# Optimization experiments

Measured on AMD Instinct MI355X. Metric: run time of the kernel, lower is better.

Reference implementation:

```python
import jax, jax.numpy as jnp
import numpy as np

# Model dims
B, S, H, E, I, K = 2, 2048, 1024, 8, 1024, 2
ALPHA, LIMIT = 1.702, 7.0  # gpt_oss activation constants (module defaults)


def setup_inputs() -> dict:
    key = jax.random.key(0)
    ks = jax.random.split(key, 5)
    sc = 0.02
    return {
        "hidden_states": jax.random.normal(ks[0], (B, S, H), jnp.float32),
        "router_weight": jax.random.normal(ks[1], (H, E), jnp.float32) * sc,
        "gate_up_proj": jax.random.normal(ks[2], (E, H, 2 * I), jnp.float32) * sc,
        "gate_up_proj_bias": jnp.zeros((E, 2 * I), jnp.float32),
        "down_proj": jax.random.normal(ks[3], (E, I, H), jnp.float32) * sc,
        "down_proj_bias": jnp.zeros((E, H), jnp.float32),
    }


def reference(hidden_states, router_weight, gate_up_proj, gate_up_proj_bias,
              down_proj, down_proj_bias):
    Bt, St, Ht = hidden_states.shape
    x = hidden_states.reshape(-1, Ht)           # [T, H], T = B*S
    T = x.shape[0]

    # Router: linear -> top-k -> softmax over selected logits (gpt_oss style)
    logits = x @ router_weight                  # [T, E]
    top_vals, top_idx = jax.lax.top_k(logits, K)
    scores = jax.nn.softmax(top_vals, axis=-1)  # [T, K]
    # Sparse combine weights: w[t, e] = score if e selected for t, else 0
    w = jnp.zeros((T, E), x.dtype).at[jnp.arange(T)[:, None], top_idx].set(scores)

    # Fused gate+up projection for every expert (dense equivalent of grouped GEMM;
    # unselected experts get zero combine weight so math matches sparse path)
    gu = jnp.einsum('th,ehf->tef', x, gate_up_proj) + gate_up_proj_bias  # [T, E, 2I]
    gate = gu[..., ::2]                         # interleaved gate (default)
    up = gu[..., 1::2]
    gate = jnp.minimum(gate, LIMIT)
    up = jnp.clip(up, -LIMIT, LIMIT)
    glu = gate * jax.nn.sigmoid(gate * ALPHA)
    act = (up + 1.0) * glu                      # [T, E, I]

    down = jnp.einsum('tei,eih->teh', act, down_proj) + down_proj_bias  # [T, E, H]

    # Weighted combine over experts (all-to-all combine is identity at D=1)
    out = jnp.einsum('te,teh->th', w, down)     # [T, H]
    return out.reshape(Bt, St, Ht)
```

## Files before the change

kernel.cpp:

```cpp
#include <hip/hip_runtime.h>
#include <hip/hip_bf16.h>
#include <cstdint>
#include <cstddef>

constexpr int T_TOK = 4096;
constexpr int H_DIM = 1024;
constexpr int E_NUM = 8;
constexpr int I_DIM = 1024;
constexpr int F2    = 2048;
constexpr float ALPHA = 1.702f;
constexpr float LIMIT = 7.0f;
constexpr int BM = 128;
constexpr int BK = 32;
constexpr int NT = 32;
constexpr int MAXT = 72;

using u16    = unsigned short;
using bf16x8 = __attribute__((ext_vector_type(8))) __bf16;
using s16x8  = __attribute__((ext_vector_type(8))) short;
using f32x4  = __attribute__((ext_vector_type(4))) float;

constexpr size_t WS_W1T  = 0;
constexpr size_t WS_DOWN = 0;
constexpr size_t WS_W2T  = 33554432;
constexpr size_t WS_ACT  = 50331648;
constexpr size_t WS_ETOK = 67108864;
constexpr size_t WS_POS  = 67239936;
constexpr size_t WS_CNT  = 67272704;
constexpr size_t WS_ROWB = 67272736;
constexpr size_t WS_ASGN = 67272768;
constexpr size_t WS_TOPE = 67273792;
constexpr size_t WS_TOPW = 67290176;
constexpr size_t WS_XBF  = 67322944;
constexpr size_t WS_NEED = 75711552;

__device__ __forceinline__ u16 f2bf(float f) {
    union { float f; unsigned u; } v; v.f = f;
    return (u16)((v.u + 0x7FFFu + ((v.u >> 16) & 1u)) >> 16);
}
__device__ __forceinline__ float bf2f(u16 u) {
    union { unsigned u; float f; } v; v.u = (unsigned)u << 16; return v.f;
}

__device__ __forceinline__ s16x8 pack8(float4 a, float4 b) {
    s16x8 r;
    r[0] = (short)f2bf(a.x); r[1] = (short)f2bf(a.y);
    r[2] = (short)f2bf(a.z); r[3] = (short)f2bf(a.w);
    r[4] = (short)f2bf(b.x); r[5] = (short)f2bf(b.y);
    r[6] = (short)f2bf(b.z); r[7] = (short)f2bf(b.w);
    return r;
}

__device__ __forceinline__ void gload16(const void* g, void* l) {
    __builtin_amdgcn_global_load_lds((const __attribute__((address_space(1))) unsigned*)g,
                                     (__attribute__((address_space(3))) unsigned*)l,
                                     16, 0, 0);
}

__device__ __forceinline__ void pipe_sync() {
    __builtin_amdgcn_sched_barrier(0);
    asm volatile("s_waitcnt vmcnt(0) lgkmcnt(0)" ::: "memory");
    __builtin_amdgcn_s_barrier();
    __builtin_amdgcn_sched_barrier(0);
}

__global__ __launch_bounds__(256) void k_xbf(const float* __restrict__ x,
                                             u16* __restrict__ xbf) {
    const size_t i = ((size_t)blockIdx.x * 256 + threadIdx.x) * 8;
    float4 a = *(const float4*)(x + i);
    float4 b = *(const float4*)(x + i + 4);
    *(s16x8*)(xbf + i) = pack8(a, b);
}

__global__ __launch_bounds__(256) void k_transpose_w1(const float* __restrict__ in,
                                                      u16* __restrict__ out) {
    __shared__ float tile[64][65];
    const int e = blockIdx.z, c0 = blockIdx.x * 64, h0 = blockIdx.y * 64;
    const int tid = threadIdx.x;
    const float* src = in + ((size_t)e * H_DIM + h0) * F2 + c0;
#pragma unroll
    for (int i = 0; i < 4; ++i) {
        int r = (tid >> 4) + i * 16, c = (tid & 15) * 4;
        float4 v = *(const float4*)(src + (size_t)r * F2 + c);
        tile[r][c] = v.x; tile[r][c + 1] = v.y; tile[r][c + 2] = v.z; tile[r][c + 3] = v.w;
    }
    __syncthreads();
    const int c = tid >> 2, hseg = (tid & 3) * 16;
    const int g = c & 1;
    const int f = (c0 + c) >> 1;
    u16* dst = out + (((size_t)e * 2 + g) * I_DIM + f) * H_DIM + h0 + hseg;
    s16x8 o0, o1;
#pragma unroll
    for (int j = 0; j < 8; ++j) o0[j] = (short)f2bf(tile[hseg + j][c]);
#pragma unroll
    for (int j = 0; j < 8; ++j) o1[j] = (short)f2bf(tile[hseg + 8 + j][c]);
    *(s16x8*)dst = o0;
    *(s16x8*)(dst + 8) = o1;
}

__global__ __launch_bounds__(256) void k_transpose_w2(const float* __restrict__ in,
                                                      u16* __restrict__ out) {
    __shared__ float tile[64][65];
    const int e = blockIdx.z, h0 = blockIdx.x * 64, i0 = blockIdx.y * 64;
    const int tid = threadIdx.x;
    const float* src = in + ((size_t)e * I_DIM + i0) * H_DIM + h0;
#pragma unroll
    for (int i = 0; i < 4; ++i) {
        int r = (tid >> 4) + i * 16, c = (tid & 15) * 4;
        float4 v = *(const float4*)(src + (size_t)r * H_DIM + c);
        tile[r][c] = v.x; tile[r][c + 1] = v.y; tile[r][c + 2] = v.z; tile[r][c + 3] = v.w;
    }
    __syncthreads();
    const int c = tid >> 2, iseg = (tid & 3) * 16;
    u16* dst = out + ((size_t)e * H_DIM + h0 + c) * I_DIM + i0 + iseg;
    s16x8 o0, o1;
#pragma unroll
    for (int j = 0; j < 8; ++j) o0[j] = (short)f2bf(tile[iseg + j][c]);
#pragma unroll
    for (int j = 0; j < 8; ++j) o1[j] = (short)f2bf(tile[iseg + 8 + j][c]);
    *(s16x8*)dst = o0;
    *(s16x8*)(dst + 8) = o1;
}

__global__ __launch_bounds__(256) void k_router_top2(const float* __restrict__ x,
                                                     const float* __restrict__ rw,
                                                     int* __restrict__ tope,
                                                     float2* __restrict__ topw) {
    const int wave = threadIdx.x >> 6, lane = threadIdx.x & 63;
    const int t = blockIdx.x * 4 + wave;
    const float* xr = x + (size_t)t * H_DIM;
    float acc[E_NUM];
#pragma unroll
    for (int e = 0; e < E_NUM; ++e) acc[e] = 0.f;
    for (int h = lane; h < H_DIM; h += 64) {
        float xv = xr[h];
        const float* r = rw + h * E_NUM;
#pragma unroll
        for (int e = 0; e < E_NUM; ++e) acc[e] += xv * r[e];
    }
#pragma unroll
    for (int e = 0; e < E_NUM; ++e) {
        float v = acc[e];
#pragma unroll
        for (int o = 32; o > 0; o >>= 1) v += __shfl_down(v, o);
        acc[e] = v;
    }
    if (lane == 0) {
        int e0 = 0; float v0 = acc[0];
#pragma unroll
        for (int e = 1; e < E_NUM; ++e) if (acc[e] > v0) { v0 = acc[e]; e0 = e; }
        int e1 = -1; float v1 = -3.4e38f;
#pragma unroll
        for (int e = 0; e < E_NUM; ++e) if (e != e0 && acc[e] > v1) { v1 = acc[e]; e1 = e; }
        float ew = expf(v1 - v0);
        float inv = 1.f / (1.f + ew);
        tope[t] = e0 | (e1 << 8);
        topw[t] = make_float2(inv, ew * inv);
    }
}

__global__ __launch_bounds__(256) void k_router_scatter(const int* __restrict__ tope,
                                                        int* __restrict__ cnt,
                                                        int* __restrict__ ent_tok,
                                                        int2* __restrict__ pos) {
    __shared__ int lcnt[E_NUM];
    __shared__ int gbase[E_NUM];
    const int tid = threadIdx.x;
    const int t = blockIdx.x * 256 + tid;
    if (tid < E_NUM) lcnt[tid] = 0;
    __syncthreads();
    const int pk = tope[t];
    const int e0 = pk & 0xff, e1 = pk >> 8;
    const int o0 = atomicAdd(&lcnt[e0], 1);
    const int o1 = atomicAdd(&lcnt[e1], 1);
    __syncthreads();
    if (tid < E_NUM) gbase[tid] = atomicAdd(&cnt[tid], lcnt[tid]);
    __syncthreads();
    const int p0 = gbase[e0] + o0;
    const int p1 = gbase[e1] + o1;
    ent_tok[e0 * T_TOK + p0] = t;
    ent_tok[e1 * T_TOK + p1] = t;
    pos[t] = make_int2(p0, p1);
}

__global__ void k_schedule(const int* __restrict__ cnt, int* __restrict__ rowbase,
                           int* __restrict__ assign) {
    if (threadIdx.x == 0) {
        int rb = 0, na = 0;
        for (int e = 0; e < E_NUM; ++e) {
            rowbase[e] = rb;
            int nt = (cnt[e] + BM - 1) >> 7;
            for (int m = 0; m < nt; ++m) assign[na++] = (e << 16) | m;
            rb += cnt[e];
        }
        for (; na < MAXT; ++na) assign[na] = -1;
    }
}

__global__ __launch_bounds__(256, 4) void k_gemm1(
    const u16* __restrict__ xbf, const u16* __restrict__ w1t,
    const float* __restrict__ bias, const int* __restrict__ ent_tok,
    const int* __restrict__ cnt, const int* __restrict__ rowbase,
    const int* __restrict__ assign, u16* __restrict__ act) {
    const int a = assign[blockIdx.y];
    if (a < 0) return;
    const int e = a >> 16, mt = a & 0xffff;
    const int j0 = blockIdx.x * 64;
    const int cs = cnt[e], r0 = mt * BM;
    __shared__ __align__(16) u16 As[2][BM * BK];
    __shared__ __align__(16) u16 Bs[2][BM * BK];
    const int tid = threadIdx.x, lane = tid & 63, wv = tid >> 6;
    const int lr = lane >> 2;
    const int sm = (lane & 3) ^ ((lr >> 1) & 3);
    const u16* asrc[2]; const u16* bsrc[2]; int dofs[2];
#pragma unroll
    for (int j = 0; j < 2; ++j) {
        const int row = wv * 32 + j * 16 + lr;
        const int aent = r0 + row;
        const int tok = (aent < cs) ? ent_tok[e * T_TOK + aent] : 0;
        asrc[j] = xbf + (size_t)tok * H_DIM + sm * 8;
        const int g = row >> 6;
        const int f = j0 + (row & 63);
        bsrc[j] = w1t + (((size_t)e * 2 + g) * I_DIM + f) * H_DIM + sm * 8;
        dofs[j] = (wv * 32 + j * 16) * BK;
    }
    const int wm = wv >> 1, wn = wv & 1;
    const int lcol = lane & 15, lk = lane >> 4;
    int aoff[4], goff[2], uoff[2];
#pragma unroll
    for (int mi = 0; mi < 4; ++mi) {
        const int r = wm * 64 + mi * 16 + lcol;
        aoff[mi] = r * 64 + ((lk ^ ((r >> 1) & 3)) << 4);
    }
#pragma unroll
    for (int nj = 0; nj < 2; ++nj) {
        const int rg_ = wn * 32 + nj * 16 + lcol;
        const int ru  = 64 + rg_;
        goff[nj] = rg_ * 64 + ((lk ^ ((rg_ >> 1) & 3)) << 4);
        uoff[nj] = ru  * 64 + ((lk ^ ((ru  >> 1) & 3)) << 4);
    }
    f32x4 ag[4][2], au[4][2];
    const f32x4 z = {0.f, 0.f, 0.f, 0.f};
#pragma unroll
    for (int mi = 0; mi < 4; ++mi) { ag[mi][0] = z; ag[mi][1] = z; au[mi][0] = z; au[mi][1] = z; }
#pragma unroll
    for (int j = 0; j < 2; ++j) {
        gload16(asrc[j], &As[0][dofs[j]]);
        gload16(bsrc[j], &Bs[0][dofs[j]]);
    }
    pipe_sync();
    int cur = 0;
    for (int t = 0; t < NT; ++t) {
        if (t + 1 < NT) {
            const int kn = (t + 1) * BK;
            u16* Ad = As[cur ^ 1]; u16* Bd = Bs[cur ^ 1];
#pragma unroll
            for (int j = 0; j < 2; ++j) {
                gload16(asrc[j] + kn, Ad + dofs[j]);
                gload16(bsrc[j] + kn, Bd + dofs[j]);
            }
        }
        const char* Ab = (const char*)As[cur];
        const char* Bb = (const char*)Bs[cur];
        bf16x8 af[4];
#pragma unroll
        for (int mi = 0; mi < 4; ++mi) af[mi] = *(const bf16x8*)(Ab + aoff[mi]);
        const bf16x8 g0 = *(const bf16x8*)(Bb + goff[0]);
        const bf16x8 g1 = *(const bf16x8*)(Bb + goff[1]);
        const bf16x8 u0 = *(const bf16x8*)(Bb + uoff[0]);
        const bf16x8 u1 = *(const bf16x8*)(Bb + uoff[1]);
#pragma unroll
        for (int mi = 0; mi < 4; ++mi) {
            ag[mi][0] = __builtin_amdgcn_mfma_f32_16x16x32_bf16(af[mi], g0, ag[mi][0], 0, 0, 0);
            au[mi][0] = __builtin_amdgcn_mfma_f32_16x16x32_bf16(af[mi], u0, au[mi][0], 0, 0, 0);
            ag[mi][1] = __builtin_amdgcn_mfma_f32_16x16x32_bf16(af[mi], g1, ag[mi][1], 0, 0, 0);
            au[mi][1] = __builtin_amdgcn_mfma_f32_16x16x32_bf16(af[mi], u1, au[mi][1], 0, 0, 0);
        }
        pipe_sync();
        cur ^= 1;
    }
    const int rbase = rowbase[e];
#pragma unroll
    for (int mi = 0; mi < 4; ++mi) {
#pragma unroll
        for (int nj = 0; nj < 2; ++nj) {
            const int col = j0 + wn * 32 + nj * 16 + lcol;
            const float bg_ = bias[e * F2 + 2 * col];
            const float bu_ = bias[e * F2 + 2 * col + 1];
#pragma unroll
            for (int rg = 0; rg < 4; ++rg) {
                const int r = wm * 64 + mi * 16 + lk * 4 + rg;
                if (r0 + r < cs) {
                    float gv = ag[mi][nj][rg] + bg_;
                    float uv = au[mi][nj][rg] + bu_;
                    gv = fminf(gv, LIMIT);
                    uv = fminf(fmaxf(uv, -LIMIT), LIMIT);
                    const float glu = gv / (1.f + expf(-ALPHA * gv));
                    act[(size_t)(rbase + r0 + r) * I_DIM + col] = f2bf((uv + 1.f) * glu);
                }
            }
        }
    }
}

__global__ __launch_bounds__(256, 4) void k_gemm2(
    const u16* __restrict__ act, const u16* __restrict__ w2t,
    const int* __restrict__ cnt, const int* __restrict__ rowbase,
    const int* __restrict__ assign, u16* __restrict__ down) {
    const int a = assign[blockIdx.y];
    if (a < 0) return;
    const int e = a >> 16, mt = a & 0xffff;
    const int n0 = blockIdx.x * 128;
    const int cs = cnt[e], r0 = mt * BM, rbase = rowbase[e];
    __shared__ __align__(16) u16 As[2][BM * BK];
    __shared__ __align__(16) u16 Bs[2][BM * BK];
    const int tid = threadIdx.x, lane = tid & 63, wv = tid >> 6;
    const int lr = lane >> 2;
    const int sm = (lane & 3) ^ ((lr >> 1) & 3);
    const u16* asrc[2]; const u16* bsrc[2]; int dofs[2];
#pragma unroll
    for (int j = 0; j < 2; ++j) {
        const int row = wv * 32 + j * 16 + lr;
        int ar = rbase + r0 + row;
        if (ar > 2 * T_TOK - 1) ar = 2 * T_TOK - 1;
        asrc[j] = act + (size_t)ar * I_DIM + sm * 8;
        bsrc[j] = w2t + ((size_t)e * H_DIM + n0 + row) * I_DIM + sm * 8;
        dofs[j] = (wv * 32 + j * 16) * BK;
    }
    const int wm = wv >> 1, wn = wv & 1;
    const int lcol = lane & 15, lk = lane >> 4;
    int aoff[4], boff[4];
#pragma unroll
    for (int mi = 0; mi < 4; ++mi) {
        const int r = wm * 64 + mi * 16 + lcol;
        const int b = wn * 64 + mi * 16 + lcol;
        aoff[mi] = r * 64 + ((lk ^ ((r >> 1) & 3)) << 4);
        boff[mi] = b * 64 + ((lk ^ ((b >> 1) & 3)) << 4);
    }
    f32x4 acc[4][4];
    const f32x4 z = {0.f, 0.f, 0.f, 0.f};
#pragma unroll
    for (int mi = 0; mi < 4; ++mi)
#pragma unroll
        for (int nj = 0; nj < 4; ++nj) acc[mi][nj] = z;
#pragma unroll
    for (int j = 0; j < 2; ++j) {
        gload16(asrc[j], &As[0][dofs[j]]);
        gload16(bsrc[j], &Bs[0][dofs[j]]);
    }
    pipe_sync();
    int cur = 0;
    for (int t = 0; t < NT; ++t) {
        if (t + 1 < NT) {
            const int kn = (t + 1) * BK;
            u16* Ad = As[cur ^ 1]; u16* Bd = Bs[cur ^ 1];
#pragma unroll
            for (int j = 0; j < 2; ++j) {
                gload16(asrc[j] + kn, Ad + dofs[j]);
                gload16(bsrc[j] + kn, Bd + dofs[j]);
            }
        }
        const char* Ab = (const char*)As[cur];
        const char* Bb = (const char*)Bs[cur];
        bf16x8 af[4], bf_[4];
#pragma unroll
        for (int mi = 0; mi < 4; ++mi) af[mi]  = *(const bf16x8*)(Ab + aoff[mi]);
#pragma unroll
        for (int nj = 0; nj < 4; ++nj) bf_[nj] = *(const bf16x8*)(Bb + boff[nj]);
#pragma unroll
        for (int mi = 0; mi < 4; ++mi)
#pragma unroll
            for (int nj = 0; nj < 4; ++nj)
                acc[mi][nj] = __builtin_amdgcn_mfma_f32_16x16x32_bf16(af[mi], bf_[nj], acc[mi][nj], 0, 0, 0);
        pipe_sync();
        cur ^= 1;
    }
#pragma unroll
    for (int mi = 0; mi < 4; ++mi) {
#pragma unroll
        for (int nj = 0; nj < 4; ++nj) {
            const int col = n0 + wn * 64 + nj * 16 + lcol;
#pragma unroll
            for (int rg = 0; rg < 4; ++rg) {
                const int r = wm * 64 + mi * 16 + lk * 4 + rg;
                if (r0 + r < cs)
                    down[(size_t)(rbase + r0 + r) * H_DIM + col] = f2bf(acc[mi][nj][rg]);
            }
        }
    }
}

__global__ __launch_bounds__(256) void k_combine(
    const int* __restrict__ tope, const float2* __restrict__ topw,
    const int2* __restrict__ pos, const int* __restrict__ rowb,
    const float* __restrict__ b2, const u16* __restrict__ down,
    float* __restrict__ out) {
    const int t = blockIdx.x;
    const int c = threadIdx.x * 4;
    const int pk = tope[t];
    const int e0 = pk & 0xff, e1 = pk >> 8;
    const int2 pp = pos[t];
    const float2 w = topw[t];
    const size_t ro0 = (size_t)(rowb[e0] + pp.x) * H_DIM;
    const size_t ro1 = (size_t)(rowb[e1] + pp.y) * H_DIM;
    ushort4 d0 = *(const ushort4*)(down + ro0 + c);
    ushort4 d1 = *(const ushort4*)(down + ro1 + c);
    float4 bb0 = *(const float4*)(b2 + e0 * H_DIM + c);
    float4 bb1 = *(const float4*)(b2 + e1 * H_DIM + c);
    float4 o;
    o.x = w.x * (bf2f(d0.x) + bb0.x) + w.y * (bf2f(d1.x) + bb1.x);
    o.y = w.x * (bf2f(d0.y) + bb0.y) + w.y * (bf2f(d1.y) + bb1.y);
    o.z = w.x * (bf2f(d0.z) + bb0.z) + w.y * (bf2f(d1.z) + bb1.z);
    o.w = w.x * (bf2f(d0.w) + bb0.w) + w.y * (bf2f(d1.w) + bb1.w);
    *(float4*)(out + (size_t)t * H_DIM + c) = o;
}

extern "C" void kernel_launch(void* const* d_in, const int* in_sizes, int n_in,
                              void* d_out, int out_size, void* d_ws, size_t ws_size,
                              hipStream_t stream) {
    const float* x   = (const float*)d_in[0];
    const float* rw  = (const float*)d_in[1];
    const float* w1  = (const float*)d_in[2];
    const float* b1  = (const float*)d_in[3];
    const float* w2  = (const float*)d_in[4];
    const float* b2  = (const float*)d_in[5];
    float* out = (float*)d_out;
    char* ws = (char*)d_ws;

    if (ws_size < WS_NEED) return;

    u16*    W1T  = (u16*)(ws + WS_W1T);
    u16*    DOWN = (u16*)(ws + WS_DOWN);
    u16*    W2T  = (u16*)(ws + WS_W2T);
    u16*    ACT  = (u16*)(ws + WS_ACT);
    int*    ETOK = (int*)(ws + WS_ETOK);
    int2*   POS  = (int2*)(ws + WS_POS);
    int*    CNT  = (int*)(ws + WS_CNT);
    int*    ROWB = (int*)(ws + WS_ROWB);
    int*    ASGN = (int*)(ws + WS_ASGN);
    int*    TOPE = (int*)(ws + WS_TOPE);
    float2* TOPW = (float2*)(ws + WS_TOPW);
    u16*    XBF  = (u16*)(ws + WS_XBF);

    hipMemsetAsync(CNT, 0, E_NUM * sizeof(int), stream);

    k_xbf<<<T_TOK * H_DIM / 2048, 256, 0, stream>>>(x, XBF);
    k_transpose_w1<<<dim3(32, 16, 8), 256, 0, stream>>>(w1, W1T);
    k_transpose_w2<<<dim3(16, 16, 8), 256, 0, stream>>>(w2, W2T);
    k_router_top2<<<T_TOK / 4, 256, 0, stream>>>(x, rw, TOPE, TOPW);
    k_router_scatter<<<T_TOK / 256, 256, 0, stream>>>(TOPE, CNT, ETOK, POS);
    k_schedule<<<1, 64, 0, stream>>>(CNT, ROWB, ASGN);
    k_gemm1<<<dim3(16, MAXT), 256, 0, stream>>>(XBF, W1T, b1, ETOK, CNT, ROWB, ASGN, ACT);
    k_gemm2<<<dim3(8, MAXT), 256, 0, stream>>>(ACT, W2T, CNT, ROWB, ASGN, DOWN);
    k_combine<<<T_TOK, 256, 0, stream>>>(TOPE, TOPW, POS, ROWB, b2, DOWN, out);
}
```

Measured before the change: 165.2 us.

## Make MoE GEMMs persistent with atomic job queue and triple-buffered loads

```diff
diff --git a/kernel.cpp b/kernel.cpp
--- a/kernel.cpp
+++ b/kernel.cpp
@@ -14,6 +14,8 @@
 constexpr int BK = 32;
 constexpr int NT = 32;
 constexpr int MAXT = 72;
+constexpr int NJOB1 = 16 * MAXT;
+constexpr int NJOB2 = 8 * MAXT;
 
 using u16    = unsigned short;
 using bf16x8 = __attribute__((ext_vector_type(8))) __bf16;
@@ -29,6 +31,7 @@
 constexpr size_t WS_CNT  = 67272704;
 constexpr size_t WS_ROWB = 67272736;
 constexpr size_t WS_ASGN = 67272768;
+constexpr size_t WS_JC   = 67273280;
 constexpr size_t WS_TOPE = 67273792;
 constexpr size_t WS_TOPW = 67290176;
 constexpr size_t WS_XBF  = 67322944;
@@ -57,12 +60,9 @@
                                      16, 0, 0);
 }
 
-__device__ __forceinline__ void pipe_sync() {
-    __builtin_amdgcn_sched_barrier(0);
-    asm volatile("s_waitcnt vmcnt(0) lgkmcnt(0)" ::: "memory");
-    __builtin_amdgcn_s_barrier();
-    __builtin_amdgcn_sched_barrier(0);
-}
+#define SB0() __builtin_amdgcn_sched_barrier(0)
+#define BARC() do { SB0(); __builtin_amdgcn_s_barrier(); SB0(); } while (0)
+#define WVM(n) do { SB0(); asm volatile("s_waitcnt vmcnt(" #n ")" ::: "memory"); } while (0)
 
 __global__ __launch_bounds__(256) void k_xbf(const float* __restrict__ x,
                                              u16* __restrict__ xbf) {
@@ -197,36 +197,21 @@
     }
 }
 
-__global__ __launch_bounds__(256, 4) void k_gemm1(
+__global__ __launch_bounds__(256, 3) void k_gemm1(
     const u16* __restrict__ xbf, const u16* __restrict__ w1t,
     const float* __restrict__ bias, const int* __restrict__ ent_tok,
     const int* __restrict__ cnt, const int* __restrict__ rowbase,
-    const int* __restrict__ assign, u16* __restrict__ act) {
-    const int a = assign[blockIdx.y];
-    if (a < 0) return;
-    const int e = a >> 16, mt = a & 0xffff;
-    const int j0 = blockIdx.x * 64;
-    const int cs = cnt[e], r0 = mt * BM;
-    __shared__ __align__(16) u16 As[2][BM * BK];
-    __shared__ __align__(16) u16 Bs[2][BM * BK];
+    const int* __restrict__ assign, int* __restrict__ jc,
+    u16* __restrict__ act) {
+    __shared__ __align__(16) u16 As[3][BM * BK];
+    __shared__ __align__(16) u16 Bs[3][BM * BK];
+    __shared__ int jobsh;
     const int tid = threadIdx.x, lane = tid & 63, wv = tid >> 6;
     const int lr = lane >> 2;
     const int sm = (lane & 3) ^ ((lr >> 1) & 3);
-    const u16* asrc[2]; const u16* bsrc[2]; int dofs[2];
-#pragma unroll
-    for (int j = 0; j < 2; ++j) {
-        const int row = wv * 32 + j * 16 + lr;
-        const int aent = r0 + row;
-        const int tok = (aent < cs) ? ent_tok[e * T_TOK + aent] : 0;
-        asrc[j] = xbf + (size_t)tok * H_DIM + sm * 8;
-        const int g = row >> 6;
-        const int f = j0 + (row & 63);
-        bsrc[j] = w1t + (((size_t)e * 2 + g) * I_DIM + f) * H_DIM + sm * 8;
-        dofs[j] = (wv * 32 + j * 16) * BK;
-    }
     const int wm = wv >> 1, wn = wv & 1;
     const int lcol = lane & 15, lk = lane >> 4;
-    int aoff[4], goff[2], uoff[2];
+    int aoff[4], goff[2], uoff[2], dofs[2];
 #pragma unroll
     for (int mi = 0; mi < 4; ++mi) {
         const int r = wm * 64 + mi * 16 + lcol;
@@ -239,97 +224,123 @@
         goff[nj] = rg_ * 64 + ((lk ^ ((rg_ >> 1) & 3)) << 4);
         uoff[nj] = ru  * 64 + ((lk ^ ((ru  >> 1) & 3)) << 4);
     }
-    f32x4 ag[4][2], au[4][2];
-    const f32x4 z = {0.f, 0.f, 0.f, 0.f};
-#pragma unroll
-    for (int mi = 0; mi < 4; ++mi) { ag[mi][0] = z; ag[mi][1] = z; au[mi][0] = z; au[mi][1] = z; }
-#pragma unroll
-    for (int j = 0; j < 2; ++j) {
-        gload16(asrc[j], &As[0][dofs[j]]);
-        gload16(bsrc[j], &Bs[0][dofs[j]]);
-    }
-    pipe_sync();
-    int cur = 0;
-    for (int t = 0; t < NT; ++t) {
-        if (t + 1 < NT) {
-            const int kn = (t + 1) * BK;
-            u16* Ad = As[cur ^ 1]; u16* Bd = Bs[cur ^ 1];
-#pragma unroll
-            for (int j = 0; j < 2; ++j) {
-                gload16(asrc[j] + kn, Ad + dofs[j]);
-                gload16(bsrc[j] + kn, Bd + dofs[j]);
+#pragma unroll
+    for (int j = 0; j < 2; ++j) dofs[j] = (wv * 32 + j * 16) * BK;
+
+    for (;;) {
+        if (tid == 0) jobsh = atomicAdd(jc, 1);
+        __syncthreads();
+        const int job = jobsh;
+        __syncthreads();
+        if (job >= NJOB1) break;
+        const int pan = job & 15, ti = job >> 4;
+        const int a = assign[ti];
+        if (a < 0) continue;
+        const int e = a >> 16, mt = a & 0xffff;
+        const int j0 = pan * 64;
+        const int cs = cnt[e], r0 = mt * BM, rbase = rowbase[e];
+
+        const u16* asrc[2]; const u16* bsrc[2];
+#pragma unroll
+        for (int j = 0; j < 2; ++j) {
+            const int row = wv * 32 + j * 16 + lr;
+            const int aent = r0 + row;
+            const int tok = (aent < cs) ? ent_tok[e * T_TOK + aent] : 0;
+            asrc[j] = xbf + (size_t)tok * H_DIM + sm * 8;
+            const int g = row >> 6;
+            const int f = j0 + (row & 63);
+            bsrc[j] = w1t + (((size_t)e * 2 + g) * I_DIM + f) * H_DIM + sm * 8;
+        }
+        f32x4 ag[4][2], au[4][2];
+        const f32x4 z = {0.f, 0.f, 0.f, 0.f};
+#pragma unroll
+        for (int mi = 0; mi < 4; ++mi) { ag[mi][0] = z; ag[mi][1] = z; au[mi][0] = z; au[mi][1] = z; }
+
+        u16 *Ar = As[0], *An = As[1], *Af = As[2];
+        u16 *Br = Bs[0], *Bn = Bs[1], *Bf = Bs[2];
+#pragma unroll
+        for (int j = 0; j < 2; ++j) {
+            gload16(asrc[j], Ar + dofs[j]);
+            gload16(bsrc[j], Br + dofs[j]);
+        }
+#pragma unroll
+        for (int j = 0; j < 2; ++j) {
+            gload16(asrc[j] + BK, An + dofs[j]);
+            gload16(bsrc[j] + BK, Bn + dofs[j]);
+        }
+        for (int t = 0; t < NT; ++t) {
+            if (t + 2 < NT) {
+                const int kn = (t + 2) * BK;
+#pragma unroll
+                for (int j = 0; j < 2; ++j) {
+                    gload16(asrc[j] + kn, Af + dofs[j]);
+                    gload16(bsrc[j] + kn, Bf + dofs[j]);
+                }
+                WVM(8);
+            } else if (t + 1 < NT) {
+                WVM(4);
+            } else {
+                WVM(0);
             }
-        }
-        const char* Ab = (const char*)As[cur];
-        const char* Bb = (const char*)Bs[cur];
-        bf16x8 af[4];
-#pragma unroll
-        for (int mi = 0; mi < 4; ++mi) af[mi] = *(const bf16x8*)(Ab + aoff[mi]);
-        const bf16x8 g0 = *(const bf16x8*)(Bb + goff[0]);
-        const bf16x8 g1 = *(const bf16x8*)(Bb + goff[1]);
-        const bf16x8 u0 = *(const bf16x8*)(Bb + uoff[0]);
-        const bf16x8 u1 = *(const bf16x8*)(Bb + uoff[1]);
+            BARC();
+            const char* Ab = (const char*)Ar;
+            const char* Bb = (const char*)Br;
+            bf16x8 af[4];
+#pragma unroll
+            for (int mi = 0; mi < 4; ++mi) af[mi] = *(const bf16x8*)(Ab + aoff[mi]);
+            const bf16x8 g0 = *(const bf16x8*)(Bb + goff[0]);
+            const bf16x8 g1 = *(const bf16x8*)(Bb + goff[1]);
+            const bf16x8 u0 = *(const bf16x8*)(Bb + uoff[0]);
+            const bf16x8 u1 = *(const bf16x8*)(Bb + uoff[1]);
+#pragma unroll
+            for (int mi = 0; mi < 4; ++mi) {
+                ag[mi][0] = __builtin_amdgcn_mfma_f32_16x16x32_bf16(af[mi], g0, ag[mi][0], 0, 0, 0);
+                au[mi][0] = __builtin_amdgcn_mfma_f32_16x16x32_bf16(af[mi], u0, au[mi][0], 0, 0, 0);
+                ag[mi][1] = __builtin_amdgcn_mfma_f32_16x16x32_bf16(af[mi], g1, ag[mi][1], 0, 0, 0);
+                au[mi][1] = __builtin_amdgcn_mfma_f32_16x16x32_bf16(af[mi], u1, au[mi][1], 0, 0, 0);
+            }
+            BARC();
+            u16* tA = Ar; Ar = An; An = Af; Af = tA;
+            u16* tB = Br; Br = Bn; Bn = Bf; Bf = tB;
+        }
 #pragma unroll
         for (int mi = 0; mi < 4; ++mi) {
-            ag[mi][0] = __builtin_amdgcn_mfma_f32_16x16x32_bf16(af[mi], g0, ag[mi][0], 0, 0, 0);
-            au[mi][0] = __builtin_amdgcn_mfma_f32_16x16x32_bf16(af[mi], u0, au[mi][0], 0, 0, 0);
-            ag[mi][1] = __builtin_amdgcn_mfma_f32_16x16x32_bf16(af[mi], g1, ag[mi][1], 0, 0, 0);
-            au[mi][1] = __builtin_amdgcn_mfma_f32_16x16x32_bf16(af[mi], u1, au[mi][1], 0, 0, 0);
-        }
-        pipe_sync();
-        cur ^= 1;
-    }
-    const int rbase = rowbase[e];
-#pragma unroll
-    for (int mi = 0; mi < 4; ++mi) {
-#pragma unroll
-        for (int nj = 0; nj < 2; ++nj) {
-            const int col = j0 + wn * 32 + nj * 16 + lcol;
-            const float bg_ = bias[e * F2 + 2 * col];
-            const float bu_ = bias[e * F2 + 2 * col + 1];
-#pragma unroll
-            for (int rg = 0; rg < 4; ++rg) {
-                const int r = wm * 64 + mi * 16 + lk * 4 + rg;
-                if (r0 + r < cs) {
-                    float gv = ag[mi][nj][rg] + bg_;
-                    float uv = au[mi][nj][rg] + bu_;
-                    gv = fminf(gv, LIMIT);
-                    uv = fminf(fmaxf(uv, -LIMIT), LIMIT);
-                    const float glu = gv / (1.f + expf(-ALPHA * gv));
-                    act[(size_t)(rbase + r0 + r) * I_DIM + col] = f2bf((uv + 1.f) * glu);
+#pragma unroll
+            for (int nj = 0; nj < 2; ++nj) {
+                const int col = j0 + wn * 32 + nj * 16 + lcol;
+                const float bg_ = bias[e * F2 + 2 * col];
+                const float bu_ = bias[e * F2 + 2 * col + 1];
+#pragma unroll
+                for (int rg = 0; rg < 4; ++rg) {
+                    const int r = wm * 64 + mi * 16 + lk * 4 + rg;
+                    if (r0 + r < cs) {
+                        float gv = ag[mi][nj][rg] + bg_;
+                        float uv = au[mi][nj][rg] + bu_;
+                        gv = fminf(gv, LIMIT);
+                        uv = fminf(fmaxf(uv, -LIMIT), LIMIT);
+                        const float glu = gv / (1.f + expf(-ALPHA * gv));
+                        act[(size_t)(rbase + r0 + r) * I_DIM + col] = f2bf((uv + 1.f) * glu);
+                    }
                 }
             }
         }
     }
 }
 
-__global__ __launch_bounds__(256, 4) void k_gemm2(
-    const u16* __restrict__ act, const u16* __restrict__ w2t,
+__global__ __launch_bounds__(256, 3) void k_gemm2(
+    const u16* __restrict__ actb, const u16* __restrict__ w2t,
     const int* __restrict__ cnt, const int* __restrict__ rowbase,
-    const int* __restrict__ assign, u16* __restrict__ down) {
-    const int a = assign[blockIdx.y];
-    if (a < 0) return;
-    const int e = a >> 16, mt = a & 0xffff;
-    const int n0 = blockIdx.x * 128;
-    const int cs = cnt[e], r0 = mt * BM, rbase = rowbase[e];
-    __shared__ __align__(16) u16 As[2][BM * BK];
-    __shared__ __align__(16) u16 Bs[2][BM * BK];
+    const int* __restrict__ assign, int* __restrict__ jc,
+    u16* __restrict__ down) {
+    __shared__ __align__(16) u16 As[3][BM * BK];
+    __shared__ __align__(16) u16 Bs[3][BM * BK];
+    __shared__ int jobsh;
     const int tid = threadIdx.x, lane = tid & 63, wv = tid >> 6;
     const int lr = lane >> 2;
     const int sm = (lane & 3) ^ ((lr >> 1) & 3);
-    const u16* asrc[2]; const u16* bsrc[2]; int dofs[2];
-#pragma unroll
-    for (int j = 0; j < 2; ++j) {
-        const int row = wv * 32 + j * 16 + lr;
-        int ar = rbase + r0 + row;
-        if (ar > 2 * T_TOK - 1) ar = 2 * T_TOK - 1;
-        asrc[j] = act + (size_t)ar * I_DIM + sm * 8;
-        bsrc[j] = w2t + ((size_t)e * H_DIM + n0 + row) * I_DIM + sm * 8;
-        dofs[j] = (wv * 32 + j * 16) * BK;
-    }
     const int wm = wv >> 1, wn = wv & 1;
     const int lcol = lane & 15, lk = lane >> 4;
-    int aoff[4], boff[4];
+    int aoff[4], boff[4], dofs[2];
 #pragma unroll
     for (int mi = 0; mi < 4; ++mi) {
         const int r = wm * 64 + mi * 16 + lcol;
@@ -337,54 +348,92 @@
         aoff[mi] = r * 64 + ((lk ^ ((r >> 1) & 3)) << 4);
         boff[mi] = b * 64 + ((lk ^ ((b >> 1) & 3)) << 4);
     }
-    f32x4 acc[4][4];
-    const f32x4 z = {0.f, 0.f, 0.f, 0.f};
-#pragma unroll
-    for (int mi = 0; mi < 4; ++mi)
-#pragma unroll
-        for (int nj = 0; nj < 4; ++nj) acc[mi][nj] = z;
-#pragma unroll
-    for (int j = 0; j < 2; ++j) {
-        gload16(asrc[j], &As[0][dofs[j]]);
-        gload16(bsrc[j], &Bs[0][dofs[j]]);
-    }
-    pipe_sync();
-    int cur = 0;
-    for (int t = 0; t < NT; ++t) {
-        if (t + 1 < NT) {
-            const int kn = (t + 1) * BK;
-            u16* Ad = As[cur ^ 1]; u16* Bd = Bs[cur ^ 1];
-#pragma unroll
-            for (int j = 0; j < 2; ++j) {
-                gload16(asrc[j] + kn, Ad + dofs[j]);
-                gload16(bsrc[j] + kn, Bd + dofs[j]);
+#pragma unroll
+    for (int j = 0; j < 2; ++j) dofs[j] = (wv * 32 + j * 16) * BK;
+
+    for (;;) {
+        if (tid == 0) jobsh = atomicAdd(jc, 1);
+        __syncthreads();
+        const int job = jobsh;
+        __syncthreads();
+        if (job >= NJOB2) break;
+        const int pan = job & 7, ti = job >> 3;
+        const int a = assign[ti];
+        if (a < 0) continue;
+        const int e = a >> 16, mt = a & 0xffff;
+        const int n0 = pan * 128;
+        const int cs = cnt[e], r0 = mt * BM, rbase = rowbase[e];
+
+        const u16* asrc[2]; const u16* bsrc[2];
+#pragma unroll
+        for (int j = 0; j < 2; ++j) {
+            const int row = wv * 32 + j * 16 + lr;
+            int ar = rbase + r0 + row;
+            if (ar > 2 * T_TOK - 1) ar = 2 * T_TOK - 1;
+            asrc[j] = actb + (size_t)ar * I_DIM + sm * 8;
+            bsrc[j] = w2t + ((size_t)e * H_DIM + n0 + row) * I_DIM + sm * 8;
+        }
+        f32x4 acc[4][4];
+        const f32x4 z = {0.f, 0.f, 0.f, 0.f};
+#pragma unroll
+        for (int mi = 0; mi < 4; ++mi)
+#pragma unroll
+            for (int nj = 0; nj < 4; ++nj) acc[mi][nj] = z;
+
+        u16 *Ar = As[0], *An = As[1], *Af = As[2];
+        u16 *Br = Bs[0], *Bn = Bs[1], *Bf = Bs[2];
+#pragma unroll
+        for (int j = 0; j < 2; ++j) {
+            gload16(asrc[j], Ar + dofs[j]);
+            gload16(bsrc[j], Br + dofs[j]);
+        }
+#pragma unroll
+        for (int j = 0; j < 2; ++j) {
+            gload16(asrc[j] + BK, An + dofs[j]);
+            gload16(bsrc[j] + BK, Bn + dofs[j]);
+        }
+        for (int t = 0; t < NT; ++t) {
+            if (t + 2 < NT) {
+                const int kn = (t + 2) * BK;
+#pragma unroll
+                for (int j = 0; j < 2; ++j) {
+                    gload16(asrc[j] + kn, Af + dofs[j]);
+                    gload16(bsrc[j] + kn, Bf + dofs[j]);
+                }
+                WVM(8);
+            } else if (t + 1 < NT) {
+                WVM(4);
+            } else {
+                WVM(0);
             }
-        }
-        const char* Ab = (const char*)As[cur];
-        const char* Bb = (const char*)Bs[cur];
-        bf16x8 af[4], bf_[4];
-#pragma unroll
-        for (int mi = 0; mi < 4; ++mi) af[mi]  = *(const bf16x8*)(Ab + aoff[mi]);
-#pragma unroll
-        for (int nj = 0; nj < 4; ++nj) bf_[nj] = *(const bf16x8*)(Bb + boff[nj]);
-#pragma unroll
-        for (int mi = 0; mi < 4; ++mi)
-#pragma unroll
-            for (int nj = 0; nj < 4; ++nj)
-                acc[mi][nj] = __builtin_amdgcn_mfma_f32_16x16x32_bf16(af[mi], bf_[nj], acc[mi][nj], 0, 0, 0);
-        pipe_sync();
-        cur ^= 1;
-    }
-#pragma unroll
-    for (int mi = 0; mi < 4; ++mi) {
-#pragma unroll
-        for (int nj = 0; nj < 4; ++nj) {
-            const int col = n0 + wn * 64 + nj * 16 + lcol;
-#pragma unroll
-            for (int rg = 0; rg < 4; ++rg) {
-                const int r = wm * 64 + mi * 16 + lk * 4 + rg;
-                if (r0 + r < cs)
-                    down[(size_t)(rbase + r0 + r) * H_DIM + col] = f2bf(acc[mi][nj][rg]);
+            BARC();
+            const char* Ab = (const char*)Ar;
+            const char* Bb = (const char*)Br;
+            bf16x8 af[4], bf_[4];
+#pragma unroll
+            for (int mi = 0; mi < 4; ++mi) af[mi]  = *(const bf16x8*)(Ab + aoff[mi]);
+#pragma unroll
+            for (int nj = 0; nj < 4; ++nj) bf_[nj] = *(const bf16x8*)(Bb + boff[nj]);
+#pragma unroll
+            for (int mi = 0; mi < 4; ++mi)
+#pragma unroll
+                for (int nj = 0; nj < 4; ++nj)
+                    acc[mi][nj] = __builtin_amdgcn_mfma_f32_16x16x32_bf16(af[mi], bf_[nj], acc[mi][nj], 0, 0, 0);
+            BARC();
+            u16* tA = Ar; Ar = An; An = Af; Af = tA;
+            u16* tB = Br; Br = Bn; Bn = Bf; Bf = tB;
+        }
+#pragma unroll
+        for (int mi = 0; mi < 4; ++mi) {
+#pragma unroll
+            for (int nj = 0; nj < 4; ++nj) {
+                const int col = n0 + wn * 64 + nj * 16 + lcol;
+#pragma unroll
+                for (int rg = 0; rg < 4; ++rg) {
+                    const int r = wm * 64 + mi * 16 + lk * 4 + rg;
+                    if (r0 + r < cs)
+                        down[(size_t)(rbase + r0 + r) * H_DIM + col] = f2bf(acc[mi][nj][rg]);
+                }
             }
         }
     }
@@ -438,11 +487,13 @@
     int*    CNT  = (int*)(ws + WS_CNT);
     int*    ROWB = (int*)(ws + WS_ROWB);
     int*    ASGN = (int*)(ws + WS_ASGN);
+    int*    JC   = (int*)(ws + WS_JC);
     int*    TOPE = (int*)(ws + WS_TOPE);
     float2* TOPW = (float2*)(ws + WS_TOPW);
     u16*    XBF  = (u16*)(ws + WS_XBF);
 
     hipMemsetAsync(CNT, 0, E_NUM * sizeof(int), stream);
+    hipMemsetAsync(JC, 0, 2 * sizeof(int), stream);
 
     k_xbf<<<T_TOK * H_DIM / 2048, 256, 0, stream>>>(x, XBF);
     k_transpose_w1<<<dim3(32, 16, 8), 256, 0, stream>>>(w1, W1T);
@@ -450,7 +501,7 @@
     k_router_top2<<<T_TOK / 4, 256, 0, stream>>>(x, rw, TOPE, TOPW);
     k_router_scatter<<<T_TOK / 256, 256, 0, stream>>>(TOPE, CNT, ETOK, POS);
     k_schedule<<<1, 64, 0, stream>>>(CNT, ROWB, ASGN);
-    k_gemm1<<<dim3(16, MAXT), 256, 0, stream>>>(XBF, W1T, b1, ETOK, CNT, ROWB, ASGN, ACT);
-    k_gemm2<<<dim3(8, MAXT), 256, 0, stream>>>(ACT, W2T, CNT, ROWB, ASGN, DOWN);
+    k_gemm1<<<768, 256, 0, stream>>>(XBF, W1T, b1, ETOK, CNT, ROWB, ASGN, JC + 0, ACT);
+    k_gemm2<<<768, 256, 0, stream>>>(ACT, W2T, CNT, ROWB, ASGN, JC + 1, DOWN);
     k_combine<<<T_TOK, 256, 0, stream>>>(TOPE, TOPW, POS, ROWB, b2, DOWN, out);
 }
```

After: 182.9 us. +10.7%, slower.

## Replace fixed grouped-GEMM grid with persistent blocks pulling tiles from per-XCD work queues

Applied to the files above, without the earlier changes.

```diff
diff --git a/kernel.cpp b/kernel.cpp
--- a/kernel.cpp
+++ b/kernel.cpp
@@ -13,7 +13,6 @@
 constexpr int BM = 128;
 constexpr int BK = 32;
 constexpr int NT = 32;
-constexpr int MAXT = 72;
 
 using u16    = unsigned short;
 using bf16x8 = __attribute__((ext_vector_type(8))) __bf16;
@@ -28,10 +27,13 @@
 constexpr size_t WS_POS  = 67239936;
 constexpr size_t WS_CNT  = 67272704;
 constexpr size_t WS_ROWB = 67272736;
-constexpr size_t WS_ASGN = 67272768;
-constexpr size_t WS_TOPE = 67273792;
-constexpr size_t WS_TOPW = 67290176;
-constexpr size_t WS_XBF  = 67322944;
+constexpr size_t WS_QC   = 67272768;
+constexpr size_t WS_QLEN = 67272832;
+constexpr size_t WS_Q1   = 67272896;
+constexpr size_t WS_Q2   = 67275456;
+constexpr size_t WS_TOPE = 67276736;
+constexpr size_t WS_TOPW = 67284928;
+constexpr size_t WS_XBF  = 67317696;
 constexpr size_t WS_NEED = 75711552;
 
 __device__ __forceinline__ u16 f2bf(float f) {
@@ -124,7 +126,7 @@
 
 __global__ __launch_bounds__(256) void k_router_top2(const float* __restrict__ x,
                                                      const float* __restrict__ rw,
-                                                     int* __restrict__ tope,
+                                                     u16* __restrict__ tope,
                                                      float2* __restrict__ topw) {
     const int wave = threadIdx.x >> 6, lane = threadIdx.x & 63;
     const int t = blockIdx.x * 4 + wave;
@@ -154,12 +156,12 @@
         for (int e = 0; e < E_NUM; ++e) if (e != e0 && acc[e] > v1) { v1 = acc[e]; e1 = e; }
         float ew = expf(v1 - v0);
         float inv = 1.f / (1.f + ew);
-        tope[t] = e0 | (e1 << 8);
+        tope[t] = (u16)(e0 | (e1 << 8));
         topw[t] = make_float2(inv, ew * inv);
     }
 }
 
-__global__ __launch_bounds__(256) void k_router_scatter(const int* __restrict__ tope,
+__global__ __launch_bounds__(256) void k_router_scatter(const u16* __restrict__ tope,
                                                         int* __restrict__ cnt,
                                                         int* __restrict__ ent_tok,
                                                         int2* __restrict__ pos) {
@@ -184,16 +186,29 @@
 }
 
 __global__ void k_schedule(const int* __restrict__ cnt, int* __restrict__ rowbase,
-                           int* __restrict__ assign) {
+                           u16* __restrict__ q1, u16* __restrict__ q2,
+                           int* __restrict__ qlen, int* __restrict__ qc) {
     if (threadIdx.x == 0) {
-        int rb = 0, na = 0;
+        int te[80], tm[80];
+        int ntiles = 0, rb = 0;
         for (int e = 0; e < E_NUM; ++e) {
             rowbase[e] = rb;
-            int nt = (cnt[e] + BM - 1) >> 7;
-            for (int m = 0; m < nt; ++m) assign[na++] = (e << 16) | m;
+            int nt = (cnt[e] + 127) >> 7;
+            for (int m = 0; m < nt; ++m) { te[ntiles] = e; tm[ntiles] = m; ++ntiles; }
             rb += cnt[e];
         }
-        for (; na < MAXT; ++na) assign[na] = -1;
+        for (int x = 0; x < 16; ++x) qc[x] = 0;
+        for (int x = 0; x < 8; ++x) {
+            int idx = 0;
+            for (int i = 0; i < ntiles; ++i)
+                for (int pp = 0; pp < 2; ++pp)
+                    q1[x * 160 + idx++] = (u16)((te[i] << 9) | (tm[i] << 4) | (x + pp * 8));
+            qlen[x] = idx;
+            int idx2 = 0;
+            for (int i = 0; i < ntiles; ++i)
+                q2[x * 80 + idx2++] = (u16)((te[i] << 9) | (tm[i] << 4) | x);
+            qlen[8 + x] = idx2;
+        }
     }
 }
 
@@ -201,32 +216,18 @@
     const u16* __restrict__ xbf, const u16* __restrict__ w1t,
     const float* __restrict__ bias, const int* __restrict__ ent_tok,
     const int* __restrict__ cnt, const int* __restrict__ rowbase,
-    const int* __restrict__ assign, u16* __restrict__ act) {
-    const int a = assign[blockIdx.y];
-    if (a < 0) return;
-    const int e = a >> 16, mt = a & 0xffff;
-    const int j0 = blockIdx.x * 64;
-    const int cs = cnt[e], r0 = mt * BM;
+    const u16* __restrict__ q1, const int* __restrict__ qlen,
+    int* __restrict__ qc, u16* __restrict__ act) {
     __shared__ __align__(16) u16 As[2][BM * BK];
     __shared__ __align__(16) u16 Bs[2][BM * BK];
+    __shared__ int jobsh;
     const int tid = threadIdx.x, lane = tid & 63, wv = tid >> 6;
     const int lr = lane >> 2;
     const int sm = (lane & 3) ^ ((lr >> 1) & 3);
-    const u16* asrc[2]; const u16* bsrc[2]; int dofs[2];
-#pragma unroll
-    for (int j = 0; j < 2; ++j) {
-        const int row = wv * 32 + j * 16 + lr;
-        const int aent = r0 + row;
-        const int tok = (aent < cs) ? ent_tok[e * T_TOK + aent] : 0;
-        asrc[j] = xbf + (size_t)tok * H_DIM + sm * 8;
-        const int g = row >> 6;
-        const int f = j0 + (row & 63);
-        bsrc[j] = w1t + (((size_t)e * 2 + g) * I_DIM + f) * H_DIM + sm * 8;
-        dofs[j] = (wv * 32 + j * 16) * BK;
-    }
     const int wm = wv >> 1, wn = wv & 1;
     const int lcol = lane & 15, lk = lane >> 4;
-    int aoff[4], goff[2], uoff[2];
+    const int q0 = blockIdx.x & 7;
+    int aoff[4], goff[2], uoff[2], dofs[2];
 #pragma unroll
     for (int mi = 0; mi < 4; ++mi) {
         const int r = wm * 64 + mi * 16 + lcol;
@@ -239,97 +240,116 @@
         goff[nj] = rg_ * 64 + ((lk ^ ((rg_ >> 1) & 3)) << 4);
         uoff[nj] = ru  * 64 + ((lk ^ ((ru  >> 1) & 3)) << 4);
     }
-    f32x4 ag[4][2], au[4][2];
-    const f32x4 z = {0.f, 0.f, 0.f, 0.f};
-#pragma unroll
-    for (int mi = 0; mi < 4; ++mi) { ag[mi][0] = z; ag[mi][1] = z; au[mi][0] = z; au[mi][1] = z; }
-#pragma unroll
-    for (int j = 0; j < 2; ++j) {
-        gload16(asrc[j], &As[0][dofs[j]]);
-        gload16(bsrc[j], &Bs[0][dofs[j]]);
-    }
-    pipe_sync();
-    int cur = 0;
-    for (int t = 0; t < NT; ++t) {
-        if (t + 1 < NT) {
-            const int kn = (t + 1) * BK;
-            u16* Ad = As[cur ^ 1]; u16* Bd = Bs[cur ^ 1];
+#pragma unroll
+    for (int j = 0; j < 2; ++j) dofs[j] = (wv * 32 + j * 16) * BK;
+
+    for (int vi = 0; vi < 8; ++vi) {
+        const int v = (q0 + vi) & 7;
+        const int len = qlen[v];
+        for (;;) {
+            __syncthreads();
+            if (tid == 0) {
+                const int cv = qc[v];
+                jobsh = (cv >= len) ? len : atomicAdd(&qc[v], 1);
+            }
+            __syncthreads();
+            if (jobsh >= len) break;
+            const int pk = q1[v * 160 + jobsh];
+            const int e = pk >> 9, mt = (pk >> 4) & 31, pan = pk & 15;
+            const int j0 = pan * 64;
+            const int cs = cnt[e], r0 = mt * BM, rbase = rowbase[e];
+
+            const u16* asrc[2]; const u16* bsrc[2];
 #pragma unroll
             for (int j = 0; j < 2; ++j) {
-                gload16(asrc[j] + kn, Ad + dofs[j]);
-                gload16(bsrc[j] + kn, Bd + dofs[j]);
+                const int row = wv * 32 + j * 16 + lr;
+                const int aent = r0 + row;
+                const int tok = (aent < cs) ? ent_tok[e * T_TOK + aent] : 0;
+                asrc[j] = xbf + (size_t)tok * H_DIM + sm * 8;
+                const int g = row >> 6;
+                const int f = j0 + (row & 63);
+                bsrc[j] = w1t + (((size_t)e * 2 + g) * I_DIM + f) * H_DIM + sm * 8;
+            }
+            f32x4 ag[4][2], au[4][2];
+            const f32x4 z = {0.f, 0.f, 0.f, 0.f};
+#pragma unroll
+            for (int mi = 0; mi < 4; ++mi) { ag[mi][0] = z; ag[mi][1] = z; au[mi][0] = z; au[mi][1] = z; }
+#pragma unroll
+            for (int j = 0; j < 2; ++j) {
+                gload16(asrc[j], &As[0][dofs[j]]);
+                gload16(bsrc[j], &Bs[0][dofs[j]]);
+            }
+            pipe_sync();
+            int cur = 0;
+            for (int t = 0; t < NT; ++t) {
+                if (t + 1 < NT) {
+                    const int kn = (t + 1) * BK;
+                    u16* Ad = As[cur ^ 1]; u16* Bd = Bs[cur ^ 1];
+#pragma unroll
+                    for (int j = 0; j < 2; ++j) {
+                        gload16(asrc[j] + kn, Ad + dofs[j]);
+                        gload16(bsrc[j] + kn, Bd + dofs[j]);
+                    }
+                }
+                const char* Ab = (const char*)As[cur];
+                const char* Bb = (const char*)Bs[cur];
+                bf16x8 af[4];
+#pragma unroll
+                for (int mi = 0; mi < 4; ++mi) af[mi] = *(const bf16x8*)(Ab + aoff[mi]);
+                const bf16x8 g0 = *(const bf16x8*)(Bb + goff[0]);
+                const bf16x8 g1 = *(const bf16x8*)(Bb + goff[1]);
+                const bf16x8 u0 = *(const bf16x8*)(Bb + uoff[0]);
+                const bf16x8 u1 = *(const bf16x8*)(Bb + uoff[1]);
+#pragma unroll
+                for (int mi = 0; mi < 4; ++mi) {
+                    ag[mi][0] = __builtin_amdgcn_mfma_f32_16x16x32_bf16(af[mi], g0, ag[mi][0], 0, 0, 0);
+                    au[mi][0] = __builtin_amdgcn_mfma_f32_16x16x32_bf16(af[mi], u0, au[mi][0], 0, 0, 0);
+                    ag[mi][1] = __builtin_amdgcn_mfma_f32_16x16x32_bf16(af[mi], g1, ag[mi][1], 0, 0, 0);
+                    au[mi][1] = __builtin_amdgcn_mfma_f32_16x16x32_bf16(af[mi], u1, au[mi][1], 0, 0, 0);
+                }
+                pipe_sync();
+                cur ^= 1;
+            }
+#pragma unroll
+            for (int mi = 0; mi < 4; ++mi) {
+#pragma unroll
+                for (int nj = 0; nj < 2; ++nj) {
+                    const int col = j0 + wn * 32 + nj * 16 + lcol;
+                    const float bg_ = bias[e * F2 + 2 * col];
+                    const float bu_ = bias[e * F2 + 2 * col + 1];
+#pragma unroll
+                    for (int rg = 0; rg < 4; ++rg) {
+                        const int r = wm * 64 + mi * 16 + lk * 4 + rg;
+                        if (r0 + r < cs) {
+                            float gv = ag[mi][nj][rg] + bg_;
+                            float uv = au[mi][nj][rg] + bu_;
+                            gv = fminf(gv, LIMIT);
+                            uv = fminf(fmaxf(uv, -LIMIT), LIMIT);
+                            const float glu = gv / (1.f + expf(-ALPHA * gv));
+                            act[(size_t)(rbase + r0 + r) * I_DIM + col] = f2bf((uv + 1.f) * glu);
+                        }
+                    }
+                }
             }
         }
-        const char* Ab = (const char*)As[cur];
-        const char* Bb = (const char*)Bs[cur];
-        bf16x8 af[4];
-#pragma unroll
-        for (int mi = 0; mi < 4; ++mi) af[mi] = *(const bf16x8*)(Ab + aoff[mi]);
-        const bf16x8 g0 = *(const bf16x8*)(Bb + goff[0]);
-        const bf16x8 g1 = *(const bf16x8*)(Bb + goff[1]);
-        const bf16x8 u0 = *(const bf16x8*)(Bb + uoff[0]);
-        const bf16x8 u1 = *(const bf16x8*)(Bb + uoff[1]);
-#pragma unroll
-        for (int mi = 0; mi < 4; ++mi) {
-            ag[mi][0] = __builtin_amdgcn_mfma_f32_16x16x32_bf16(af[mi], g0, ag[mi][0], 0, 0, 0);
-            au[mi][0] = __builtin_amdgcn_mfma_f32_16x16x32_bf16(af[mi], u0, au[mi][0], 0, 0, 0);
-            ag[mi][1] = __builtin_amdgcn_mfma_f32_16x16x32_bf16(af[mi], g1, ag[mi][1], 0, 0, 0);
-            au[mi][1] = __builtin_amdgcn_mfma_f32_16x16x32_bf16(af[mi], u1, au[mi][1], 0, 0, 0);
-        }
-        pipe_sync();
-        cur ^= 1;
-    }
-    const int rbase = rowbase[e];
-#pragma unroll
-    for (int mi = 0; mi < 4; ++mi) {
-#pragma unroll
-        for (int nj = 0; nj < 2; ++nj) {
-            const int col = j0 + wn * 32 + nj * 16 + lcol;
-            const float bg_ = bias[e * F2 + 2 * col];
-            const float bu_ = bias[e * F2 + 2 * col + 1];
-#pragma unroll
-            for (int rg = 0; rg < 4; ++rg) {
-                const int r = wm * 64 + mi * 16 + lk * 4 + rg;
-                if (r0 + r < cs) {
-                    float gv = ag[mi][nj][rg] + bg_;
-                    float uv = au[mi][nj][rg] + bu_;
-                    gv = fminf(gv, LIMIT);
-                    uv = fminf(fmaxf(uv, -LIMIT), LIMIT);
-                    const float glu = gv / (1.f + expf(-ALPHA * gv));
-                    act[(size_t)(rbase + r0 + r) * I_DIM + col] = f2bf((uv + 1.f) * glu);
-                }
-            }
-        }
     }
 }
 
 __global__ __launch_bounds__(256, 4) void k_gemm2(
-    const u16* __restrict__ act, const u16* __restrict__ w2t,
+    const u16* __restrict__ actb, const u16* __restrict__ w2t,
     const int* __restrict__ cnt, const int* __restrict__ rowbase,
-    const int* __restrict__ assign, u16* __restrict__ down) {
-    const int a = assign[blockIdx.y];
-    if (a < 0) return;
-    const int e = a >> 16, mt = a & 0xffff;
-    const int n0 = blockIdx.x * 128;
-    const int cs = cnt[e], r0 = mt * BM, rbase = rowbase[e];
+    const u16* __restrict__ q2, const int* __restrict__ qlen,
+    int* __restrict__ qc, u16* __restrict__ down) {
     __shared__ __align__(16) u16 As[2][BM * BK];
     __shared__ __align__(16) u16 Bs[2][BM * BK];
+    __shared__ int jobsh;
     const int tid = threadIdx.x, lane = tid & 63, wv = tid >> 6;
     const int lr = lane >> 2;
     const int sm = (lane & 3) ^ ((lr >> 1) & 3);
-    const u16* asrc[2]; const u16* bsrc[2]; int dofs[2];
-#pragma unroll
-    for (int j = 0; j < 2; ++j) {
-        const int row = wv * 32 + j * 16 + lr;
-        int ar = rbase + r0 + row;
-        if (ar > 2 * T_TOK - 1) ar = 2 * T_TOK - 1;
-        asrc[j] = act + (size_t)ar * I_DIM + sm * 8;
-        bsrc[j] = w2t + ((size_t)e * H_DIM + n0 + row) * I_DIM + sm * 8;
-        dofs[j] = (wv * 32 + j * 16) * BK;
-    }
     const int wm = wv >> 1, wn = wv & 1;
     const int lcol = lane & 15, lk = lane >> 4;
-    int aoff[4], boff[4];
+    const int q0 = blockIdx.x & 7;
+    int aoff[4], boff[4], dofs[2];
 #pragma unroll
     for (int mi = 0; mi < 4; ++mi) {
         const int r = wm * 64 + mi * 16 + lcol;
@@ -337,61 +357,91 @@
         aoff[mi] = r * 64 + ((lk ^ ((r >> 1) & 3)) << 4);
         boff[mi] = b * 64 + ((lk ^ ((b >> 1) & 3)) << 4);
     }
-    f32x4 acc[4][4];
-    const f32x4 z = {0.f, 0.f, 0.f, 0.f};
-#pragma unroll
-    for (int mi = 0; mi < 4; ++mi)
-#pragma unroll
-        for (int nj = 0; nj < 4; ++nj) acc[mi][nj] = z;
-#pragma unroll
-    for (int j = 0; j < 2; ++j) {
-        gload16(asrc[j], &As[0][dofs[j]]);
-        gload16(bsrc[j], &Bs[0][dofs[j]]);
-    }
-    pipe_sync();
-    int cur = 0;
-    for (int t = 0; t < NT; ++t) {
-        if (t + 1 < NT) {
-            const int kn = (t + 1) * BK;
-            u16* Ad = As[cur ^ 1]; u16* Bd = Bs[cur ^ 1];
+#pragma unroll
+    for (int j = 0; j < 2; ++j) dofs[j] = (wv * 32 + j * 16) * BK;
+
+    for (int vi = 0; vi < 8; ++vi) {
+        const int v = (q0 + vi) & 7;
+        const int len = qlen[8 + v];
+        for (;;) {
+            __syncthreads();
+            if (tid == 0) {
+                const int cv = qc[8 + v];
+                jobsh = (cv >= len) ? len : atomicAdd(&qc[8 + v], 1);
+            }
+            __syncthreads();
+            if (jobsh >= len) break;
+            const int pk = q2[v * 80 + jobsh];
+            const int e = pk >> 9, mt = (pk >> 4) & 31, pan = pk & 15;
+            const int n0 = pan * 128;
+            const int cs = cnt[e], r0 = mt * BM, rbase = rowbase[e];
+
+            const u16* asrc[2]; const u16* bsrc[2];
 #pragma unroll
             for (int j = 0; j < 2; ++j) {
-                gload16(asrc[j] + kn, Ad + dofs[j]);
-                gload16(bsrc[j] + kn, Bd + dofs[j]);
+                const int row = wv * 32 + j * 16 + lr;
+                int ar = rbase + r0 + row;
+                if (ar > 2 * T_TOK - 1) ar = 2 * T_TOK - 1;
+                asrc[j] = actb + (size_t)ar * I_DIM + sm * 8;
+                bsrc[j] = w2t + ((size_t)e * H_DIM + n0 + row) * I_DIM + sm * 8;
+            }
+            f32x4 acc[4][4];
+            const f32x4 z = {0.f, 0.f, 0.f, 0.f};
+#pragma unroll
+            for (int mi = 0; mi < 4; ++mi)
+#pragma unroll
+                for (int nj = 0; nj < 4; ++nj) acc[mi][nj] = z;
+#pragma unroll
+            for (int j = 0; j < 2; ++j) {
+                gload16(asrc[j], &As[0][dofs[j]]);
+                gload16(bsrc[j], &Bs[0][dofs[j]]);
+            }
+            pipe_sync();
+            int cur = 0;
+            for (int t = 0; t < NT; ++t) {
+                if (t + 1 < NT) {
+                    const int kn = (t + 1) * BK;
+                    u16* Ad = As[cur ^ 1]; u16* Bd = Bs[cur ^ 1];
+#pragma unroll
+                    for (int j = 0; j < 2; ++j) {
+                        gload16(asrc[j] + kn, Ad + dofs[j]);
+                        gload16(bsrc[j] + kn, Bd + dofs[j]);
+                    }
+                }
+                const char* Ab = (const char*)As[cur];
+                const char* Bb = (const char*)Bs[cur];
+                bf16x8 af[4], bf_[4];
+#pragma unroll
+                for (int mi = 0; mi < 4; ++mi) af[mi]  = *(const bf16x8*)(Ab + aoff[mi]);
+#pragma unroll
+                for (int nj = 0; nj < 4; ++nj) bf_[nj] = *(const bf16x8*)(Bb + boff[nj]);
+#pragma unroll
+                for (int mi = 0; mi < 4; ++mi)
+#pragma unroll
+                    for (int nj = 0; nj < 4; ++nj)
+                        acc[mi][nj] = __builtin_amdgcn_mfma_f32_16x16x32_bf16(af[mi], bf_[nj], acc[mi][nj], 0, 0, 0);
+                pipe_sync();
+                cur ^= 1;
+            }
+#pragma unroll
+            for (int mi = 0; mi < 4; ++mi) {
+#pragma unroll
+                for (int nj = 0; nj < 4; ++nj) {
+                    const int col = n0 + wn * 64 + nj * 16 + lcol;
+#pragma unroll
+                    for (int rg = 0; rg < 4; ++rg) {
+                        const int r = wm * 64 + mi * 16 + lk * 4 + rg;
+                        if (r0 + r < cs)
+                            down[(size_t)(rbase + r0 + r) * H_DIM + col] = f2bf(acc[mi][nj][rg]);
+                    }
+                }
             }
         }
-        const char* Ab = (const char*)As[cur];
-        const char* Bb = (const char*)Bs[cur];
-        bf16x8 af[4], bf_[4];
-#pragma unroll
-        for (int mi = 0; mi < 4; ++mi) af[mi]  = *(const bf16x8*)(Ab + aoff[mi]);
-#pragma unroll
-        for (int nj = 0; nj < 4; ++nj) bf_[nj] = *(const bf16x8*)(Bb + boff[nj]);
-#pragma unroll
-        for (int mi = 0; mi < 4; ++mi)
-#pragma unroll
-            for (int nj = 0; nj < 4; ++nj)
-                acc[mi][nj] = __builtin_amdgcn_mfma_f32_16x16x32_bf16(af[mi], bf_[nj], acc[mi][nj], 0, 0, 0);
-        pipe_sync();
-        cur ^= 1;
-    }
-#pragma unroll
-    for (int mi = 0; mi < 4; ++mi) {
-#pragma unroll
-        for (int nj = 0; nj < 4; ++nj) {
-            const int col = n0 + wn * 64 + nj * 16 + lcol;
-#pragma unroll
-            for (int rg = 0; rg < 4; ++rg) {
-                const int r = wm * 64 + mi * 16 + lk * 4 + rg;
-                if (r0 + r < cs)
-                    down[(size_t)(rbase + r0 + r) * H_DIM + col] = f2bf(acc[mi][nj][rg]);
-            }
-        }
     }
 }
 
 __global__ __launch_bounds__(256) void k_combine(
-    const int* __restrict__ tope, const float2* __restrict__ topw,
+    const u16* __restrict__ tope, const float2* __restrict__ topw,
     const int2* __restrict__ pos, const int* __restrict__ rowb,
     const float* __restrict__ b2, const u16* __restrict__ down,
     float* __restrict__ out) {
@@ -437,8 +487,11 @@
     int2*   POS  = (int2*)(ws + WS_POS);
     int*    CNT  = (int*)(ws + WS_CNT);
     int*    ROWB = (int*)(ws + WS_ROWB);
-    int*    ASGN = (int*)(ws + WS_ASGN);
-    int*    TOPE = (int*)(ws + WS_TOPE);
+    int*    QC   = (int*)(ws + WS_QC);
+    int*    QLEN = (int*)(ws + WS_QLEN);
+    u16*    Q1   = (u16*)(ws + WS_Q1);
+    u16*    Q2   = (u16*)(ws + WS_Q2);
+    u16*    TOPE = (u16*)(ws + WS_TOPE);
     float2* TOPW = (float2*)(ws + WS_TOPW);
     u16*    XBF  = (u16*)(ws + WS_XBF);
 
@@ -449,8 +502,8 @@
     k_transpose_w2<<<dim3(16, 16, 8), 256, 0, stream>>>(w2, W2T);
     k_router_top2<<<T_TOK / 4, 256, 0, stream>>>(x, rw, TOPE, TOPW);
     k_router_scatter<<<T_TOK / 256, 256, 0, stream>>>(TOPE, CNT, ETOK, POS);
-    k_schedule<<<1, 64, 0, stream>>>(CNT, ROWB, ASGN);
-    k_gemm1<<<dim3(16, MAXT), 256, 0, stream>>>(XBF, W1T, b1, ETOK, CNT, ROWB, ASGN, ACT);
-    k_gemm2<<<dim3(8, MAXT), 256, 0, stream>>>(ACT, W2T, CNT, ROWB, ASGN, DOWN);
+    k_schedule<<<1, 64, 0, stream>>>(CNT, ROWB, Q1, Q2, QLEN, QC);
+    k_gemm1<<<1024, 256, 0, stream>>>(XBF, W1T, b1, ETOK, CNT, ROWB, Q1, QLEN, QC, ACT);
+    k_gemm2<<<1024, 256, 0, stream>>>(ACT, W2T, CNT, ROWB, Q2, QLEN, QC, DOWN);
     k_combine<<<T_TOK, 256, 0, stream>>>(TOPE, TOPW, POS, ROWB, b2, DOWN, out);
 }
```

Measured after the change: 295.3 us. 1.79x slower.
